# Performance work log

Hardware: AMD Instinct MI355X
Metric: run time of the kernel (lower is better)

Reference implementation:

```python
import jax, jax.numpy as jnp
import numpy as np

H, W = 200, 200            # image_size
X_RANGE = (0.0, 100.0)
Y_RANGE = (0.0, 100.0)
SIZE = 36                   # kernel 'size' from source
SIGMA = 3.0
K = SIZE + 1                # kernel is 37x37 (arange(-18, 19))


def _gaussian_kernel():
    r = jnp.arange(-(SIZE // 2), SIZE // 2 + 1, dtype=jnp.float32)
    k1 = jnp.exp(-(r ** 2) / (2.0 * SIGMA ** 2))
    k2 = k1[:, None] * k1[None, :]
    return k2 / k2.sum()    # [K, K]


def setup_inputs() -> dict:
    key = jax.random.key(0)
    # trajectory coords in world units [0, 100) -> spread over whole map
    x_t = jax.random.uniform(key, (512, 64, 2), dtype=jnp.float32) * 100.0
    return {"x_t": x_t}


def reference(x_t):
    B, T, _ = x_t.shape
    x_scale = W / (X_RANGE[1] - X_RANGE[0])
    y_scale = H / (Y_RANGE[1] - Y_RANGE[0])
    # .long() in torch truncates toward zero; inputs are >= 0 here so astype(int32) matches
    x_pix = ((x_t[:, :, 0] - X_RANGE[0]) * x_scale).astype(jnp.int32)   # [B, T]
    y_pix = H - ((x_t[:, :, 1] - Y_RANGE[0]) * y_scale).astype(jnp.int32)
    valid = ~(jnp.isnan(x_t[:, :, 0]) | jnp.isnan(x_t[:, :, 1]))        # [B, T]

    half = SIZE // 2
    x_start = jnp.clip(x_pix - half, 0, W - SIZE)
    y_start = jnp.clip(y_pix - half, 0, H - SIZE)
    x_end = jnp.clip(x_pix + half, 0, W)
    y_end = jnp.clip(y_pix + half, 0, H)
    kx = x_end - x_start    # patch width  (<= 36, kernel[:,:kx] = top-left slice)
    ky = y_end - y_start    # patch height

    kern = _gaussian_kernel()                       # [K, K]
    r = jnp.arange(K)
    c = jnp.arange(K)
    # mask: kernel[:ky, :kx] slice, and point validity            [B, T, K, K]
    mask = ((r[None, None, :, None] < ky[..., None, None])
            & (c[None, None, None, :] < kx[..., None, None])
            & valid[..., None, None])
    vals = jnp.where(mask, kern[None, None, :, :], 0.0)            # [B, T, K, K]
    rows = jnp.clip(y_start[..., None, None] + r[None, None, :, None], 0, H - 1)
    cols = jnp.clip(x_start[..., None, None] + c[None, None, None, :], 0, W - 1)
    rows = jnp.broadcast_to(rows, (B, T, K, K))
    cols = jnp.broadcast_to(cols, (B, T, K, K))
    flat = (rows * W + cols).reshape(B, -1)                        # [B, T*K*K]

    # parallel scatter-add splat of all Gaussian patches
    heat = jnp.zeros((B, H * W), jnp.float32)
    heat = heat.at[jnp.arange(B)[:, None], flat].add(vals.reshape(B, -1))
    heat = heat.reshape(B, H, W)

    # per-image max normalization (max over dim1 then dim2 == max over both)
    m = heat.max(axis=(1, 2), keepdims=True)
    return heat / (m + 1e-10)
```

## Files before the change

kernel.cpp:

```cpp
#include <hip/hip_runtime.h>


#define NT 64
#define BLK 448
#define TDIM 224
#define NTL 7

typedef short bf16x8 __attribute__((ext_vector_type(8)));
typedef float f32x16 __attribute__((ext_vector_type(16)));

static __device__ inline unsigned short f2bf(float f) {
    unsigned int u = __float_as_uint(f);
    u = (u + 0x7FFFu + ((u >> 16) & 1u)) >> 16;
    return (unsigned short)u;
}

struct __align__(16) SMem {
    unsigned short Rm[TDIM][64];
    unsigned short Cm[TDIM][64];
    unsigned short k1b[40];
    float wmax[NTL];
};

__global__ __launch_bounds__(BLK) void heatmap_kernel(const float* __restrict__ x_t,
                                                      float* __restrict__ out) {
    __shared__ SMem s;
    const int tid  = threadIdx.x;
    const int lane = tid & 63;
    const int wv   = tid >> 6;
    const int b    = blockIdx.x;

    if (tid < 37) {
        float sum = 0.0f, mine = 0.0f;
        #pragma unroll
        for (int i = 0; i < 37; ++i) {
            float r = (float)(i - 18);
            float v = expf(-(r * r) * (1.0f / 18.0f));
            sum += v;
            if (i == tid) mine = v;
        }
        s.k1b[tid] = f2bf(mine / sum);
    }
    __syncthreads();

    {
        const int q  = tid & 31;
        const int r0 = tid >> 5;
        float4 pxy = *(const float4*)(x_t + (size_t)b * NT * 2 + 4 * q);
        bool v0 = (pxy.x == pxy.x) && (pxy.y == pxy.y);
        int xp0 = (int)(pxy.x * 2.0f), yp0 = 200 - (int)(pxy.y * 2.0f);
        int xs0 = min(max(xp0 - 18, 0), 164), ys0 = min(max(yp0 - 18, 0), 164);
        int kx0 = v0 ? (min(max(xp0 + 18, 0), 200) - xs0) : 0;
        int ky0 = v0 ? (min(max(yp0 + 18, 0), 200) - ys0) : 0;
        bool v1 = (pxy.z == pxy.z) && (pxy.w == pxy.w);
        int xp1 = (int)(pxy.z * 2.0f), yp1 = 200 - (int)(pxy.w * 2.0f);
        int xs1 = min(max(xp1 - 18, 0), 164), ys1 = min(max(yp1 - 18, 0), 164);
        int kx1 = v1 ? (min(max(xp1 + 18, 0), 200) - xs1) : 0;
        int ky1 = v1 ? (min(max(yp1 + 18, 0), 200) - ys1) : 0;

        #pragma unroll
        for (int i = 0; i < 16; ++i) {
            int row = r0 + 14 * i;
            int sw  = (4 * q) ^ ((row & 7) << 4);
            int d0 = row - ys0, d1 = row - ys1;
            unsigned a0 = ((unsigned)d0 < (unsigned)ky0) ? s.k1b[d0] : 0u;
            unsigned a1 = ((unsigned)d1 < (unsigned)ky1) ? s.k1b[d1] : 0u;
            *(unsigned*)((char*)s.Rm + row * 128 + sw) = a0 | (a1 << 16);
            int e0 = row - xs0, e1 = row - xs1;
            unsigned c0 = ((unsigned)e0 < (unsigned)kx0) ? s.k1b[e0] : 0u;
            unsigned c1 = ((unsigned)e1 < (unsigned)kx1) ? s.k1b[e1] : 0u;
            *(unsigned*)((char*)s.Cm + row * 128 + sw) = c0 | (c1 << 16);
        }
    }
    __syncthreads();

    const int swl = (lane & 7) << 4;

    bf16x8 A[4];
    {
        const char* ab = (const char*)s.Rm + (wv * 32 + (lane & 31)) * 128;
        #pragma unroll
        for (int m = 0; m < 4; ++m)
            A[m] = *(const bf16x8*)(ab + ((16 * (2 * m + (lane >> 5))) ^ swl));
    }

    f32x16 acc[NTL];
    #pragma unroll
    for (int tx = 0; tx < NTL; ++tx) {
        #pragma unroll
        for (int r = 0; r < 16; ++r) acc[tx][r] = 0.0f;
    }
    #pragma unroll
    for (int tx = 0; tx < NTL; ++tx) {
        const char* bb = (const char*)s.Cm + (tx * 32 + (lane & 31)) * 128;
        #pragma unroll
        for (int m = 0; m < 4; ++m) {
            bf16x8 B = *(const bf16x8*)(bb + ((16 * (2 * m + (lane >> 5))) ^ swl));
            acc[tx] = __builtin_amdgcn_mfma_f32_32x32x16_bf16(A[m], B, acc[tx], 0, 0, 0);
        }
    }

    float gmax = 0.0f;
    #pragma unroll
    for (int tx = 0; tx < NTL; ++tx) {
        #pragma unroll
        for (int r = 0; r < 16; ++r) gmax = fmaxf(gmax, acc[tx][r]);
    }
    #pragma unroll
    for (int off = 32; off > 0; off >>= 1) gmax = fmaxf(gmax, __shfl_xor(gmax, off));
    if (lane == 0) s.wmax[wv] = gmax;
    __syncthreads();
    float mm = s.wmax[0];
    #pragma unroll
    for (int w = 1; w < NTL; ++w) mm = fmaxf(mm, s.wmax[w]);
    const float scale = 1.0f / (mm + 1e-10f);

    float* ob = out + (size_t)b * (200 * 200);
    const int colbase = lane & 31;
    const int rowoff  = wv * 32 + 4 * (lane >> 5);
    #pragma unroll
    for (int tx = 0; tx < NTL; ++tx) {
        const int gcol = tx * 32 + colbase;
        #pragma unroll
        for (int r = 0; r < 16; ++r) {
            int grow = rowoff + (r & 3) + 8 * (r >> 2);
            if (grow < 200 && gcol < 200)
                ob[grow * 200 + gcol] = acc[tx][r] * scale;
        }
    }
}

extern "C" void kernel_launch(void* const* d_in, const int* in_sizes, int n_in,
                              void* d_out, int out_size, void* d_ws, size_t ws_size,
                              hipStream_t stream) {
    const float* x_t = (const float*)d_in[0];
    float* out = (float*)d_out;
    const int B = in_sizes[0] / (NT * 2);
    heatmap_kernel<<<B, BLK, 0, stream>>>(x_t, out);
}
```

Before: 28.75 us.

## Swap MFMA operands for float4 stores and recompute tiles instead of holding accumulators

Swaps the A/B operands of the MFMA so each lane's accumulator holds consecutive output columns, which allows float4 vectorized global stores instead of scalar stores. It also recomputes the MFMA tiles in a second pass rather than keeping 7 accumulator tiles live, which cuts register pressure. The shared-memory kernel table and its sync are removed, with each thread computing Gaussian weights inline for 4 points. This doubles the MFMA work and adds more exp calls in exchange for wider stores and fewer registers.

Measured after the change: 27.58 us. -4.1%, faster.

```diff
diff --git a/kernel.cpp b/kernel.cpp
--- a/kernel.cpp
+++ b/kernel.cpp
@@ -2,23 +2,22 @@
 
 
 #define NT 64
-#define BLK 448
 #define TDIM 224
 #define NTL 7
+#define BLK 448
 
 typedef short bf16x8 __attribute__((ext_vector_type(8)));
 typedef float f32x16 __attribute__((ext_vector_type(16)));
 
-static __device__ inline unsigned short f2bf(float f) {
+static __device__ inline unsigned f2bf(float f) {
     unsigned int u = __float_as_uint(f);
     u = (u + 0x7FFFu + ((u >> 16) & 1u)) >> 16;
-    return (unsigned short)u;
+    return u & 0xFFFFu;
 }
 
 struct __align__(16) SMem {
     unsigned short Rm[TDIM][64];
     unsigned short Cm[TDIM][64];
-    unsigned short k1b[40];
     float wmax[NTL];
 };
 
@@ -30,81 +29,79 @@
     const int wv   = tid >> 6;
     const int b    = blockIdx.x;
 
-    if (tid < 37) {
-        float sum = 0.0f, mine = 0.0f;
-        #pragma unroll
-        for (int i = 0; i < 37; ++i) {
-            float r = (float)(i - 18);
-            float v = expf(-(r * r) * (1.0f / 18.0f));
-            sum += v;
-            if (i == tid) mine = v;
-        }
-        s.k1b[tid] = f2bf(mine / sum);
+    float ssum = 0.0f;
+    #pragma unroll
+    for (int i = 0; i < 37; ++i) {
+        float r = (float)(i - 18);
+        ssum += expf(-(r * r) * (1.0f / 18.0f));
     }
-    __syncthreads();
+    const float invs = 1.0f / ssum;
 
     {
-        const int q  = tid & 31;
-        const int r0 = tid >> 5;
-        float4 pxy = *(const float4*)(x_t + (size_t)b * NT * 2 + 4 * q);
-        bool v0 = (pxy.x == pxy.x) && (pxy.y == pxy.y);
-        int xp0 = (int)(pxy.x * 2.0f), yp0 = 200 - (int)(pxy.y * 2.0f);
-        int xs0 = min(max(xp0 - 18, 0), 164), ys0 = min(max(yp0 - 18, 0), 164);
-        int kx0 = v0 ? (min(max(xp0 + 18, 0), 200) - xs0) : 0;
-        int ky0 = v0 ? (min(max(yp0 + 18, 0), 200) - ys0) : 0;
-        bool v1 = (pxy.z == pxy.z) && (pxy.w == pxy.w);
-        int xp1 = (int)(pxy.z * 2.0f), yp1 = 200 - (int)(pxy.w * 2.0f);
-        int xs1 = min(max(xp1 - 18, 0), 164), ys1 = min(max(yp1 - 18, 0), 164);
-        int kx1 = v1 ? (min(max(xp1 + 18, 0), 200) - xs1) : 0;
-        int ky1 = v1 ? (min(max(yp1 + 18, 0), 200) - ys1) : 0;
-
+        const int q4 = tid & 15;
+        const int rg = tid >> 4;
+        const float4 p01 = *(const float4*)(x_t + (size_t)b * 128 + 8 * q4);
+        const float4 p23 = *(const float4*)(x_t + (size_t)b * 128 + 8 * q4 + 4);
+        float px[4] = {p01.x, p01.z, p23.x, p23.z};
+        float py[4] = {p01.y, p01.w, p23.y, p23.w};
+        int xs[4], ys[4], kx[4], ky[4];
         #pragma unroll
-        for (int i = 0; i < 16; ++i) {
-            int row = r0 + 14 * i;
-            int sw  = (4 * q) ^ ((row & 7) << 4);
-            int d0 = row - ys0, d1 = row - ys1;
-            unsigned a0 = ((unsigned)d0 < (unsigned)ky0) ? s.k1b[d0] : 0u;
-            unsigned a1 = ((unsigned)d1 < (unsigned)ky1) ? s.k1b[d1] : 0u;
-            *(unsigned*)((char*)s.Rm + row * 128 + sw) = a0 | (a1 << 16);
-            int e0 = row - xs0, e1 = row - xs1;
-            unsigned c0 = ((unsigned)e0 < (unsigned)kx0) ? s.k1b[e0] : 0u;
-            unsigned c1 = ((unsigned)e1 < (unsigned)kx1) ? s.k1b[e1] : 0u;
-            *(unsigned*)((char*)s.Cm + row * 128 + sw) = c0 | (c1 << 16);
+        for (int k = 0; k < 4; ++k) {
+            bool valid = (px[k] == px[k]) && (py[k] == py[k]);
+            int xp = (int)(px[k] * 2.0f);
+            int yp = 200 - (int)(py[k] * 2.0f);
+            xs[k] = min(max(xp - 18, 0), 164);
+            ys[k] = min(max(yp - 18, 0), 164);
+            kx[k] = valid ? (min(max(xp + 18, 0), 200) - xs[k]) : 0;
+            ky[k] = valid ? (min(max(yp + 18, 0), 200) - ys[k]) : 0;
+        }
+        #pragma unroll
+        for (int i = 0; i < 8; ++i) {
+            const int row = rg + 28 * i;
+            const int off = (8 * q4) ^ ((row & 7) << 4);
+            unsigned rv[4], cv[4];
+            #pragma unroll
+            for (int k = 0; k < 4; ++k) {
+                int d = row - ys[k];
+                float fd = (float)(d - 18);
+                float v = expf(-(fd * fd) * (1.0f / 18.0f)) * invs;
+                rv[k] = ((unsigned)d < (unsigned)ky[k]) ? f2bf(v) : 0u;
+                int e = row - xs[k];
+                float fe = (float)(e - 18);
+                float w = expf(-(fe * fe) * (1.0f / 18.0f)) * invs;
+                cv[k] = ((unsigned)e < (unsigned)kx[k]) ? f2bf(w) : 0u;
+            }
+            uint2 R = {rv[0] | (rv[1] << 16), rv[2] | (rv[3] << 16)};
+            *(uint2*)((char*)s.Rm + row * 128 + off) = R;
+            uint2 C = {cv[0] | (cv[1] << 16), cv[2] | (cv[3] << 16)};
+            *(uint2*)((char*)s.Cm + row * 128 + off) = C;
         }
     }
     __syncthreads();
 
     const int swl = (lane & 7) << 4;
 
-    bf16x8 A[4];
+    bf16x8 Bf[4];
     {
-        const char* ab = (const char*)s.Rm + (wv * 32 + (lane & 31)) * 128;
+        const char* rb = (const char*)s.Rm + (wv * 32 + (lane & 31)) * 128;
         #pragma unroll
         for (int m = 0; m < 4; ++m)
-            A[m] = *(const bf16x8*)(ab + ((16 * (2 * m + (lane >> 5))) ^ swl));
-    }
-
-    f32x16 acc[NTL];
-    #pragma unroll
-    for (int tx = 0; tx < NTL; ++tx) {
-        #pragma unroll
-        for (int r = 0; r < 16; ++r) acc[tx][r] = 0.0f;
-    }
-    #pragma unroll
-    for (int tx = 0; tx < NTL; ++tx) {
-        const char* bb = (const char*)s.Cm + (tx * 32 + (lane & 31)) * 128;
-        #pragma unroll
-        for (int m = 0; m < 4; ++m) {
-            bf16x8 B = *(const bf16x8*)(bb + ((16 * (2 * m + (lane >> 5))) ^ swl));
-            acc[tx] = __builtin_amdgcn_mfma_f32_32x32x16_bf16(A[m], B, acc[tx], 0, 0, 0);
-        }
+            Bf[m] = *(const bf16x8*)(rb + ((16 * (2 * m + (lane >> 5))) ^ swl));
     }
 
     float gmax = 0.0f;
-    #pragma unroll
     for (int tx = 0; tx < NTL; ++tx) {
+        const char* ab = (const char*)s.Cm + (tx * 32 + (lane & 31)) * 128;
+        f32x16 acc;
         #pragma unroll
-        for (int r = 0; r < 16; ++r) gmax = fmaxf(gmax, acc[tx][r]);
+        for (int r = 0; r < 16; ++r) acc[r] = 0.0f;
+        #pragma unroll
+        for (int m = 0; m < 4; ++m) {
+            bf16x8 Af = *(const bf16x8*)(ab + ((16 * (2 * m + (lane >> 5))) ^ swl));
+            acc = __builtin_amdgcn_mfma_f32_32x32x16_bf16(Af, Bf[m], acc, 0, 0, 0);
+        }
+        #pragma unroll
+        for (int r = 0; r < 16; ++r) gmax = fmaxf(gmax, acc[r]);
     }
     #pragma unroll
     for (int off = 32; off > 0; off >>= 1) gmax = fmaxf(gmax, __shfl_xor(gmax, off));
@@ -116,16 +113,28 @@
     const float scale = 1.0f / (mm + 1e-10f);
 
     float* ob = out + (size_t)b * (200 * 200);
-    const int colbase = lane & 31;
-    const int rowoff  = wv * 32 + 4 * (lane >> 5);
-    #pragma unroll
+    const int y  = wv * 32 + (lane & 31);
+    const int xh = 4 * (lane >> 5);
     for (int tx = 0; tx < NTL; ++tx) {
-        const int gcol = tx * 32 + colbase;
+        const char* ab = (const char*)s.Cm + (tx * 32 + (lane & 31)) * 128;
+        f32x16 acc;
         #pragma unroll
-        for (int r = 0; r < 16; ++r) {
-            int grow = rowoff + (r & 3) + 8 * (r >> 2);
-            if (grow < 200 && gcol < 200)
-                ob[grow * 200 + gcol] = acc[tx][r] * scale;
+        for (int r = 0; r < 16; ++r) acc[r] = 0.0f;
+        #pragma unroll
+        for (int m = 0; m < 4; ++m) {
+            bf16x8 Af = *(const bf16x8*)(ab + ((16 * (2 * m + (lane >> 5))) ^ swl));
+            acc = __builtin_amdgcn_mfma_f32_32x32x16_bf16(Af, Bf[m], acc, 0, 0, 0);
+        }
+        if (y < 200) {
+            #pragma unroll
+            for (int g = 0; g < 4; ++g) {
+                const int x0 = tx * 32 + 8 * g + xh;
+                if (x0 < 200) {
+                    float4 v = {acc[4 * g] * scale, acc[4 * g + 1] * scale,
+                                acc[4 * g + 2] * scale, acc[4 * g + 3] * scale};
+                    *(float4*)(ob + (size_t)y * 200 + x0) = v;
+                }
+            }
         }
     }
 }
```
